# Optimization experiments

Measured on AMD Instinct MI355X. Metric: run time of the kernel, lower is better.

## Reference

```python
import jax, jax.numpy as jnp
import numpy as np

N, E, IN, H0, H1 = 50000, 1600000, 64, 64, 128


def _gcn(h, W, b, row, col):
    # PyG GCNConv, add_self_loops=False, unit edge weights:
    # out[col] += d^{-1/2}[row] * d^{-1/2}[col] * (h @ W)[row]; bias added after aggregation
    n = h.shape[0]
    deg = jnp.zeros((n,), h.dtype).at[col].add(jnp.ones((row.shape[0],), h.dtype))
    dinv = jnp.where(deg > 0, jax.lax.rsqrt(jnp.maximum(deg, 1e-12)), 0.0)
    norm = (dinv[row] * dinv[col])[:, None]  # [E,1]
    m = h @ W  # transform before propagate (small GEMM)
    out = jnp.zeros((n, W.shape[1]), h.dtype).at[col].add(norm * m[row])
    return out + b


def _bn(h, g, b):
    # BatchNorm1d training-mode math (biased variance), eps=1e-5
    mu = h.mean(0)
    var = ((h - mu) ** 2).mean(0)
    return g * (h - mu) * jax.lax.rsqrt(var + 1e-5) + b


def _san(h):
    return jnp.nan_to_num(h, nan=0.0, posinf=100.0, neginf=-100.0)


def _slice(x, ei, W0, b0, W1, b1, res1, g0, be0, g1, be1):
    row, col = ei[0], ei[1]
    # layer 0: conv -> bn -> relu -> (dropout=eval identity) -> residual (Identity, 64==64) -> nan_to_num
    h1 = _san(jax.nn.relu(_bn(_gcn(x, W0, b0, row, col), g0, be0)) + x)
    # layer 1 (last): conv -> bn -> residual (Linear proj 64->128, no bias) -> nan_to_num
    h2 = _san(_bn(_gcn(h1, W1, b1, row, col), g1, be1) + h1 @ res1)
    return h2


def setup_inputs() -> dict:
    k = jax.random.split(jax.random.key(0), 16)
    f = lambda kk, sh, s: jax.random.normal(kk, sh, jnp.float32) * s
    return {
        "x": f(k[0], (N, IN), 1.0),
        "edge_index0": jax.random.randint(k[1], (2, E), 0, N),
        "edge_index1": jax.random.randint(k[2], (2, E), 0, N),
        "w0_s0": f(k[3], (IN, H0), 0.1), "b0_s0": jnp.zeros((H0,), jnp.float32),
        "w1_s0": f(k[4], (H0, H1), 0.1), "b1_s0": jnp.zeros((H1,), jnp.float32),
        "res1_s0": f(k[5], (H0, H1), 0.1),
        "w0_s1": f(k[6], (IN, H0), 0.1), "b0_s1": jnp.zeros((H0,), jnp.float32),
        "w1_s1": f(k[7], (H0, H1), 0.1), "b1_s1": jnp.zeros((H1,), jnp.float32),
        "res1_s1": f(k[8], (H0, H1), 0.1),
        "bn_g0": jnp.ones((H0,), jnp.float32), "bn_b0": jnp.zeros((H0,), jnp.float32),
        "bn_g1": jnp.ones((H1,), jnp.float32), "bn_b1": jnp.zeros((H1,), jnp.float32),
        "fc1_w": f(k[9], (2 * H1, H1), 0.1), "fc1_b": jnp.zeros((H1,), jnp.float32),
        "fc2_w": f(k[10], (H1, 2), 0.1), "fc2_b": jnp.zeros((2,), jnp.float32),
    }


def reference(x, edge_index0, edge_index1,
              w0_s0, b0_s0, w1_s0, b1_s0, res1_s0,
              w0_s1, b0_s1, w1_s1, b1_s1, res1_s1,
              bn_g0, bn_b0, bn_g1, bn_b1,
              fc1_w, fc1_b, fc2_w, fc2_b):
    out0 = _slice(x, edge_index0, w0_s0, b0_s0, w1_s0, b1_s0, res1_s0, bn_g0, bn_b0, bn_g1, bn_b1)
    out1 = _slice(x, edge_index1, w0_s1, b0_s1, w1_s1, b1_s1, res1_s1, bn_g0, bn_b0, bn_g1, bn_b1)
    combined = jnp.concatenate([out0, out1], axis=1)  # [N, 2*H1]
    h = jax.nn.relu(combined @ fc1_w + fc1_b)  # dropout is eval-mode identity
    logits = h @ fc2_w + fc2_b
    return logits, jax.nn.softmax(logits, axis=1)
```

## Files before the change

kernel.cpp:

```cpp
#include <hip/hip_runtime.h>
#include <hip/hip_bf16.h>
#include <math.h>


typedef short v8s __attribute__((ext_vector_type(8)));
typedef float f32x4 __attribute__((ext_vector_type(4)));

#define BSTRIDE 10240

__device__ __forceinline__ float sanf(float v) {
    if (v != v) return 0.f;
    if (isinf(v)) return v > 0.f ? 100.f : -100.f;
    return v;
}

__device__ __forceinline__ unsigned short bf16of(float v) {
    __hip_bfloat16 h = __float2bfloat16(v);
    return *(unsigned short*)&h;
}
__device__ __forceinline__ unsigned pack2(float lo, float hi) {
    return (unsigned)bf16of(lo) | ((unsigned)bf16of(hi) << 16);
}
__device__ __forceinline__ float uflo(unsigned u) { return __uint_as_float(u << 16); }
__device__ __forceinline__ float ufhi(unsigned u) { return __uint_as_float(u & 0xFFFF0000u); }
__device__ __forceinline__ float fofbf16(unsigned short u) {
    return __uint_as_float(((unsigned)u) << 16);
}

__device__ __forceinline__ void packone(const float* __restrict__ src, unsigned* __restrict__ dst,
                                        int L, int Khalf, int F) {
    int c = L / Khalf, kp = L - c * Khalf;
    dst[L] = pack2(src[(2 * kp) * F + c], src[(2 * kp + 1) * F + c]);
}

__global__ __launch_bounds__(256) void prep_kernel(const float* __restrict__ w0_0,
                                                   const float* __restrict__ w0_1,
                                                   const float* __restrict__ w1_0,
                                                   const float* __restrict__ w1_1,
                                                   const float* __restrict__ r_0,
                                                   const float* __restrict__ r_1,
                                                   const float* __restrict__ fc1,
                                                   const float* __restrict__ x,
                                                   unsigned* __restrict__ wpk,
                                                   int* __restrict__ bcnt,
                                                   float* __restrict__ sums,
                                                   unsigned short* __restrict__ xb, int n64) {
    int gid = blockIdx.x * 256 + threadIdx.x;
    if (gid < 512) bcnt[gid] = 0;
    if (gid < 8192) sums[gid] = 0.f;
    if (gid < 2048)       packone(w0_0, wpk + 0,     gid - 0,     32, 64);
    else if (gid < 4096)  packone(w0_1, wpk + 2048,  gid - 2048,  32, 64);
    else if (gid < 8192)  packone(w1_0, wpk + 4096,  gid - 4096,  32, 128);
    else if (gid < 12288) packone(w1_1, wpk + 8192,  gid - 8192,  32, 128);
    else if (gid < 16384) packone(r_0,  wpk + 12288, gid - 12288, 32, 128);
    else if (gid < 20480) packone(r_1,  wpk + 16384, gid - 16384, 32, 128);
    else if (gid < 36864) packone(fc1,  wpk + 20480, gid - 20480, 128, 128);
    if (gid < n64) xb[gid] = bf16of(x[gid]);
}


__global__ __launch_bounds__(512) void kC_bin(const int* __restrict__ ei0,
                                              const int* __restrict__ ei1,
                                              int* __restrict__ bcnt,
                                              unsigned* __restrict__ binned,
                                              int E, int n) {
    __shared__ int cnt[512];
    __shared__ int base[512];
    int t = threadIdx.x;
    cnt[t] = 0;
    int E2 = 2 * E;
    int e0 = blockIdx.x * 8192;
    unsigned pk[16];
    int bk[16];
    __syncthreads();
#pragma unroll
    for (int j = 0; j < 16; ++j) {
        int ge = e0 + t + j * 512;
        bk[j] = -1;
        if (ge < E2) {
            int slice = ge >= E;
            const int* ei = slice ? ei1 : ei0;
            int e = ge - slice * E;
            int col = ei[E + e], row = ei[e];
            int gcol = slice * n + col;
            bk[j] = gcol >> 8;
            pk[j] = (unsigned)row | (((unsigned)gcol & 255u) << 16);
            atomicAdd(&cnt[bk[j]], 1);
        }
    }
    __syncthreads();
    {
        int c = cnt[t];
        base[t] = c ? atomicAdd(&bcnt[t], c) : 0;
    }
    __syncthreads();
    cnt[t] = 0;
    __syncthreads();
#pragma unroll
    for (int j = 0; j < 16; ++j) {
        if (bk[j] >= 0) {
            int loc = atomicAdd(&cnt[bk[j]], 1);
            int off = base[bk[j]] + loc;
            if (off < BSTRIDE) binned[(size_t)bk[j] * BSTRIDE + off] = pk[j];
        }
    }
}

__global__ __launch_bounds__(256) void kB_scan(const int* __restrict__ bcnt,
                                               int* __restrict__ bstart, int NB) {
    __shared__ int tmp[256];
    int t = threadIdx.x, carry = 0;
    for (int bse = 0; bse < NB; bse += 256) {
        int i = bse + t;
        int v = (i < NB) ? bcnt[i] : 0;
        tmp[t] = v;
        __syncthreads();
        for (int off = 1; off < 256; off <<= 1) {
            int u = (t >= off) ? tmp[t - off] : 0;
            __syncthreads();
            tmp[t] += u;
            __syncthreads();
        }
        if (i < NB) bstart[i] = tmp[t] - v + carry;
        carry += tmp[255];
        __syncthreads();
    }
    if (t == 0) bstart[NB] = carry;
}

__global__ __launch_bounds__(512) void kD_build(const unsigned* __restrict__ binned,
                                                const int* __restrict__ bstart,
                                                int* __restrict__ rowptr,
                                                float* __restrict__ dinv,
                                                unsigned short* __restrict__ csr,
                                                int n2, int NB) {
    __shared__ int cnt[256];
    __shared__ int scn[256];
    __shared__ int cur[256];
    int b = blockIdx.x, t = threadIdx.x;
    int s = bstart[b], e = bstart[b + 1];
    int m = e - s;
    const unsigned* seg = binned + (size_t)b * BSTRIDE;
    if (t < 256) cnt[t] = 0;
    __syncthreads();
    for (int i = t; i < m; i += 512) atomicAdd(&cnt[(seg[i] >> 16) & 255], 1);
    __syncthreads();
    int v = (t < 256) ? cnt[t] : 0;
    if (t < 256) scn[t] = v;
    __syncthreads();
    for (int off = 1; off < 256; off <<= 1) {
        int u = (t < 256 && t >= off) ? scn[t - off] : 0;
        __syncthreads();
        if (t < 256) scn[t] += u;
        __syncthreads();
    }
    if (t < 256) {
        int excl = scn[t] - v;
        int gcol = b * 256 + t;
        if (gcol < n2) {
            rowptr[gcol] = s + excl;
            dinv[gcol] = v > 0 ? rsqrtf((float)v) : 0.f;
        }
        cur[t] = excl;
    }
    __syncthreads();
    for (int i = t; i < m; i += 512) {
        unsigned p = seg[i];
        int cl = (p >> 16) & 255;
        int pos = s + atomicAdd(&cur[cl], 1);
        csr[pos] = (unsigned short)(p & 0xFFFFu);
    }
    if (b == 0 && t == 0) rowptr[n2] = bstart[NB];
}

template <int F>
__global__ __launch_bounds__(256) void gg_kernel(const int* __restrict__ rowptr,
                                                 const unsigned short* __restrict__ csr,
                                                 const unsigned short* __restrict__ mtab,
                                                 size_t slice_stride,
                                                 const float* __restrict__ dinv,
                                                 const unsigned* __restrict__ WT0,
                                                 const unsigned* __restrict__ WT1,
                                                 unsigned short* __restrict__ Cb,
                                                 float* __restrict__ sums_base,
                                                 int roff, int n) {
    constexpr int NC = F / 16;
    __shared__ unsigned As32[64 * 36];
    __shared__ float ls[2 * F];
    int BPS = (n + 63) >> 6;
    int slice = blockIdx.x >= BPS;
    int sb = blockIdx.x - slice * BPS;
    int row0 = slice * n + sb * 64;
    int rows = min(64, n - sb * 64);
    for (int i = threadIdx.x; i < 2 * F; i += 256) ls[i] = 0.f;
    int w = threadIdx.x >> 6, lane = threadIdx.x & 63;
    int l = lane & 7;
    const unsigned short* mb = mtab + slice_stride * slice;
    const float* dsrc = dinv + slice * n;
#pragma unroll
    for (int p = 0; p < 2; ++p) {
        int nl = 16 * w + p * 8 + (lane >> 3);
        float a0 = 0.f, a1 = 0.f, a2 = 0.f, a3 = 0.f, a4 = 0.f, a5 = 0.f, a6 = 0.f, a7 = 0.f;
        if (nl < rows) {
            int node = row0 + nl;
            int s = rowptr[node], e = rowptr[node + 1];
            int b = s;
            for (; b + 8 <= e; b += 8) {
                int idx = csr[b + l];
                float wsrc = dsrc[idx];
                uint4 u[8];
                float ws[8];
#pragma unroll
                for (int j = 0; j < 8; ++j) {
                    int r = __shfl(idx, j, 8);
                    ws[j] = __shfl(wsrc, j, 8);
                    u[j] = *(const uint4*)&mb[(size_t)r * 64 + l * 8];
                }
#pragma unroll
                for (int j = 0; j < 8; ++j) {
                    a0 = fmaf(ws[j], uflo(u[j].x), a0);
                    a1 = fmaf(ws[j], ufhi(u[j].x), a1);
                    a2 = fmaf(ws[j], uflo(u[j].y), a2);
                    a3 = fmaf(ws[j], ufhi(u[j].y), a3);
                    a4 = fmaf(ws[j], uflo(u[j].z), a4);
                    a5 = fmaf(ws[j], ufhi(u[j].z), a5);
                    a6 = fmaf(ws[j], uflo(u[j].w), a6);
                    a7 = fmaf(ws[j], ufhi(u[j].w), a7);
                }
            }
            if (b < e) {
                int cntn = e - b;
                int idx = (b + l < e) ? (int)csr[b + l] : 0;
                float wsrc = dsrc[idx];
                for (int j = 0; j < cntn; ++j) {
                    int r = __shfl(idx, j, 8);
                    float wj = __shfl(wsrc, j, 8);
                    uint4 u = *(const uint4*)&mb[(size_t)r * 64 + l * 8];
                    a0 = fmaf(wj, uflo(u.x), a0);
                    a1 = fmaf(wj, ufhi(u.x), a1);
                    a2 = fmaf(wj, uflo(u.y), a2);
                    a3 = fmaf(wj, ufhi(u.y), a3);
                    a4 = fmaf(wj, uflo(u.z), a4);
                    a5 = fmaf(wj, ufhi(u.z), a5);
                    a6 = fmaf(wj, uflo(u.w), a6);
                    a7 = fmaf(wj, ufhi(u.w), a7);
                }
            }
            float d = dinv[node];
            a0 *= d; a1 *= d; a2 *= d; a3 *= d;
            a4 *= d; a5 *= d; a6 *= d; a7 *= d;
        }
        uint4 o;
        o.x = pack2(a0, a1);
        o.y = pack2(a2, a3);
        o.z = pack2(a4, a5);
        o.w = pack2(a6, a7);
        *(uint4*)&As32[nl * 36 + l * 4] = o;
    }
    __syncthreads();
    const unsigned* WT = slice ? WT1 : WT0;
    int q = lane >> 4, ln = lane & 15;
    v8s af0 = *(const v8s*)&As32[(16 * w + ln) * 36 + q * 4];
    v8s af1 = *(const v8s*)&As32[(16 * w + ln) * 36 + 16 + q * 4];
    f32x4 acc[NC];
#pragma unroll
    for (int ct = 0; ct < NC; ++ct) acc[ct] = {0.f, 0.f, 0.f, 0.f};
#pragma unroll
    for (int ct = 0; ct < NC; ++ct) {
        v8s b0 = *(const v8s*)&WT[(ct * 16 + ln) * 32 + q * 4];
        v8s b1 = *(const v8s*)&WT[(ct * 16 + ln) * 32 + 16 + q * 4];
        acc[ct] = __builtin_amdgcn_mfma_f32_16x16x32_bf16(af0, b0, acc[ct], 0, 0, 0);
        acc[ct] = __builtin_amdgcn_mfma_f32_16x16x32_bf16(af1, b1, acc[ct], 0, 0, 0);
    }
#pragma unroll
    for (int ct = 0; ct < NC; ++ct) {
        float s1 = 0.f, s2 = 0.f;
#pragma unroll
        for (int i = 0; i < 4; ++i) {
            int r = 16 * w + q * 4 + i;
            if (r < rows) {
                float v = acc[ct][i];
                Cb[(size_t)(row0 + r) * F + ct * 16 + ln] = bf16of(v);
                s1 += v;
                s2 += v * v;
            }
        }
        s1 += __shfl_xor(s1, 16); s1 += __shfl_xor(s1, 32);
        s2 += __shfl_xor(s2, 16); s2 += __shfl_xor(s2, 32);
        if (q == 0) {
            atomicAdd(&ls[ct * 16 + ln], s1);
            atomicAdd(&ls[F + ct * 16 + ln], s2);
        }
    }
    __syncthreads();
    if (threadIdx.x < F) {
        float* dst = sums_base + (blockIdx.x & 7) * 1024 + roff + slice * 2 * F;
        unsafeAtomicAdd(&dst[threadIdx.x], ls[threadIdx.x]);
        unsafeAtomicAdd(&dst[F + threadIdx.x], ls[F + threadIdx.x]);
    }
}


__global__ __launch_bounds__(256) void apply0_kernel(const unsigned short* __restrict__ t0b,
                                                     const float* __restrict__ x,
                                                     const float* __restrict__ sums_base,
                                                     int roff,
                                                     const float* __restrict__ g,
                                                     const float* __restrict__ be,
                                                     unsigned short* __restrict__ h1b,
                                                     int n64, int n) {
    __shared__ float sc[128];
    int i0 = blockIdx.x * 256;
    int slice = i0 >= n64;
    int t = threadIdx.x;
    if (t < 64) {
        float s1 = 0.f, s2 = 0.f;
#pragma unroll
        for (int r = 0; r < 8; ++r) {
            const float* src = sums_base + r * 1024 + roff + slice * 128;
            s1 += src[t];
            s2 += src[64 + t];
        }
        float inv_n = 1.0f / (float)n;
        float mu = s1 * inv_n;
        float var = fmaxf(s2 * inv_n - mu * mu, 0.f);
        float scale = g[t] * rsqrtf(var + 1e-5f);
        sc[t] = scale;
        sc[64 + t] = be[t] - mu * scale;
    }
    __syncthreads();
    int i = i0 + t;
    int f = i & 63;
    float v = fmaf(fofbf16(t0b[i]), sc[f], sc[64 + f]);
    v = fmaxf(v, 0.f) + x[i - slice * n64];
    h1b[i] = bf16of(sanf(v));
}

__global__ __launch_bounds__(256) void mfma_apply1(const unsigned short* __restrict__ h1b,
                                                   const unsigned short* __restrict__ Tb,
                                                   const unsigned* __restrict__ RT0,
                                                   const unsigned* __restrict__ RT1,
                                                   const float* __restrict__ sums_base,
                                                   const float* __restrict__ g,
                                                   const float* __restrict__ be,
                                                   unsigned short* __restrict__ comb, int n) {
    __shared__ float sc[256];
    int BPS = (n + 63) >> 6;
    int slice = blockIdx.x >= BPS;
    int sb = blockIdx.x - slice * BPS;
    int row0 = slice * n + sb * 64;
    int rows = min(64, n - sb * 64);
    int t = threadIdx.x;
    if (t < 128) {
        float s1 = 0.f, s2 = 0.f;
#pragma unroll
        for (int r = 0; r < 8; ++r) {
            const float* src = sums_base + r * 1024 + slice * 256;
            s1 += src[t];
            s2 += src[128 + t];
        }
        float inv_n = 1.0f / (float)n;
        float mu = s1 * inv_n;
        float var = fmaxf(s2 * inv_n - mu * mu, 0.f);
        float scale = g[t] * rsqrtf(var + 1e-5f);
        sc[t] = scale;
        sc[128 + t] = be[t] - mu * scale;
    }
    __syncthreads();
    const unsigned* WT = slice ? RT1 : RT0;
    int w = t >> 6, lane = t & 63, q = lane >> 4, ln = lane & 15;
    const unsigned* A32 = (const unsigned*)h1b;
    size_t arow = (size_t)(row0 + 16 * w + ln) * 32;
    v8s af0 = *(const v8s*)&A32[arow + q * 4];
    v8s af1 = *(const v8s*)&A32[arow + 16 + q * 4];
    f32x4 acc[8];
#pragma unroll
    for (int ct = 0; ct < 8; ++ct) acc[ct] = {0.f, 0.f, 0.f, 0.f};
#pragma unroll
    for (int ct = 0; ct < 8; ++ct) {
        v8s b0 = *(const v8s*)&WT[(ct * 16 + ln) * 32 + q * 4];
        v8s b1 = *(const v8s*)&WT[(ct * 16 + ln) * 32 + 16 + q * 4];
        acc[ct] = __builtin_amdgcn_mfma_f32_16x16x32_bf16(af0, b0, acc[ct], 0, 0, 0);
        acc[ct] = __builtin_amdgcn_mfma_f32_16x16x32_bf16(af1, b1, acc[ct], 0, 0, 0);
    }
#pragma unroll
    for (int ct = 0; ct < 8; ++ct) {
        int c = ct * 16 + ln;
        float scale = sc[c], shift = sc[128 + c];
#pragma unroll
        for (int i = 0; i < 4; ++i) {
            int r = 16 * w + q * 4 + i;
            if (r >= rows) continue;
            int row = row0 + r;
            float tv = fofbf16(Tb[(size_t)row * 128 + c]);
            float o = sanf(fmaf(tv, scale, shift) + acc[ct][i]);
            comb[(size_t)(row - slice * n) * 256 + slice * 128 + c] = bf16of(o);
        }
    }
}

__global__ __launch_bounds__(256) void mfma_head_fc2(const unsigned short* __restrict__ comb,
                                                     const unsigned* __restrict__ FT,
                                                     const float* __restrict__ bias,
                                                     const float* __restrict__ w2,
                                                     const float* __restrict__ b2,
                                                     float* __restrict__ out, int n) {
    int row0 = blockIdx.x * 64;
    int rows = min(64, n - row0);
    int w = threadIdx.x >> 6, lane = threadIdx.x & 63, q = lane >> 4, ln = lane & 15;
    const unsigned* A32 = (const unsigned*)comb;
    size_t arow = (size_t)(row0 + 16 * w + ln) * 128;
    f32x4 acc[8];
#pragma unroll
    for (int ct = 0; ct < 8; ++ct) acc[ct] = {0.f, 0.f, 0.f, 0.f};
#pragma unroll
    for (int kt = 0; kt < 4; ++kt) {
        v8s af0 = *(const v8s*)&A32[arow + kt * 32 + q * 4];
        v8s af1 = *(const v8s*)&A32[arow + kt * 32 + 16 + q * 4];
#pragma unroll
        for (int ct = 0; ct < 8; ++ct) {
            v8s b0 = *(const v8s*)&FT[(ct * 16 + ln) * 128 + kt * 32 + q * 4];
            v8s b1 = *(const v8s*)&FT[(ct * 16 + ln) * 128 + kt * 32 + 16 + q * 4];
            acc[ct] = __builtin_amdgcn_mfma_f32_16x16x32_bf16(af0, b0, acc[ct], 0, 0, 0);
            acc[ct] = __builtin_amdgcn_mfma_f32_16x16x32_bf16(af1, b1, acc[ct], 0, 0, 0);
        }
    }
    float p0[4] = {0.f, 0.f, 0.f, 0.f}, p1[4] = {0.f, 0.f, 0.f, 0.f};
#pragma unroll
    for (int ct = 0; ct < 8; ++ct) {
        int c = ct * 16 + ln;
        float bi = bias[c];
        float w20 = w2[c * 2], w21 = w2[c * 2 + 1];
#pragma unroll
        for (int i = 0; i < 4; ++i) {
            float h = fmaxf(acc[ct][i] + bi, 0.f);
            p0[i] = fmaf(h, w20, p0[i]);
            p1[i] = fmaf(h, w21, p1[i]);
        }
    }
#pragma unroll
    for (int i = 0; i < 4; ++i) {
#pragma unroll
        for (int msk = 1; msk < 16; msk <<= 1) {
            p0[i] += __shfl_xor(p0[i], msk);
            p1[i] += __shfl_xor(p1[i], msk);
        }
    }
    if (ln == 0) {
        float bb0 = b2[0], bb1 = b2[1];
#pragma unroll
        for (int i = 0; i < 4; ++i) {
            int r = 16 * w + q * 4 + i;
            if (r >= rows) continue;
            int R = row0 + r;
            float l0 = p0[i] + bb0, l1 = p1[i] + bb1;
            float mx = fmaxf(l0, l1);
            float e0 = expf(l0 - mx), e1 = expf(l1 - mx);
            float inv = 1.0f / (e0 + e1);
            out[(size_t)R * 2] = l0;
            out[(size_t)R * 2 + 1] = l1;
            out[(size_t)2 * n + R * 2] = e0 * inv;
            out[(size_t)2 * n + R * 2 + 1] = e1 * inv;
        }
    }
}

static inline int cdiv(int a, int b) { return (a + b - 1) / b; }

extern "C" void kernel_launch(void* const* d_in, const int* in_sizes, int n_in,
                              void* d_out, int out_size, void* d_ws, size_t ws_size,
                              hipStream_t stream) {
    const float* x       = (const float*)d_in[0];
    const int*   ei0     = (const int*)d_in[1];
    const int*   ei1     = (const int*)d_in[2];
    const float* w0_s0   = (const float*)d_in[3];
    const float* w1_s0   = (const float*)d_in[5];
    const float* res1_s0 = (const float*)d_in[7];
    const float* w0_s1   = (const float*)d_in[8];
    const float* w1_s1   = (const float*)d_in[10];
    const float* res1_s1 = (const float*)d_in[12];
    const float* bn_g0   = (const float*)d_in[13];
    const float* bn_b0   = (const float*)d_in[14];
    const float* bn_g1   = (const float*)d_in[15];
    const float* bn_b1   = (const float*)d_in[16];
    const float* fc1_w   = (const float*)d_in[17];
    const float* fc1_b   = (const float*)d_in[18];
    const float* fc2_w   = (const float*)d_in[19];
    const float* fc2_b   = (const float*)d_in[20];
    float* out = (float*)d_out;

    int n = in_sizes[0] / 64;
    int E = in_sizes[1] / 2;
    int n2 = 2 * n, E2 = 2 * E;
    int n64 = n * 64;
    int NB = cdiv(n2, 256);
    int BPS = cdiv(n, 64);

    unsigned short* Tb   = (unsigned short*)d_ws;
    unsigned short* h1b  = Tb + (size_t)n2 * 128;
    unsigned short* comb = h1b + (size_t)n2 * 64;
    unsigned short* xb   = comb + (size_t)n * 256;
    float* dinv = (float*)(xb + (size_t)n * 64);
    float* sums = dinv + n2;
    unsigned* wpk = (unsigned*)(sums + 8192);
    unsigned short* csr = (unsigned short*)(wpk + 36864);
    int* rowptr = (int*)(csr + (size_t)E2);
    int* bcnt   = rowptr + (n2 + 1);
    int* bstart = bcnt + 512;
    unsigned short* t0b = Tb;
    unsigned* binned = (unsigned*)comb;
    unsigned* w0T0 = wpk + 0,    *w0T1 = wpk + 2048;
    unsigned* w1T0 = wpk + 4096, *w1T1 = wpk + 8192;
    unsigned* rT0  = wpk + 12288,*rT1  = wpk + 16384;
    unsigned* fT   = wpk + 20480;

    prep_kernel<<<cdiv(n64, 256), 256, 0, stream>>>(w0_s0, w0_s1, w1_s0, w1_s1,
                                                    res1_s0, res1_s1, fc1_w, x,
                                                    wpk, bcnt, sums, xb, n64);
    kC_bin<<<cdiv(E2, 8192), 512, 0, stream>>>(ei0, ei1, bcnt, binned, E, n);
    kB_scan<<<1, 256, 0, stream>>>(bcnt, bstart, NB);
    kD_build<<<NB, 512, 0, stream>>>(binned, bstart, rowptr, dinv, csr, n2, NB);

    gg_kernel<64><<<2 * BPS, 256, 0, stream>>>(rowptr, csr, xb, 0, dinv,
                                               w0T0, w0T1, t0b, sums, 512, n);
    apply0_kernel<<<2 * n64 / 256, 256, 0, stream>>>(t0b, x, sums, 512, bn_g0, bn_b0,
                                                     h1b, n64, n);

    gg_kernel<128><<<2 * BPS, 256, 0, stream>>>(rowptr, csr, h1b, (size_t)n * 64, dinv,
                                                w1T0, w1T1, Tb, sums, 0, n);
    mfma_apply1<<<2 * BPS, 256, 0, stream>>>(h1b, Tb, rT0, rT1, sums, bn_g1, bn_b1,
                                             comb, n);

    mfma_head_fc2<<<BPS, 256, 0, stream>>>(comb, fT, fc1_b, fc2_w, fc2_b, out, n);
}
```

Before: 408.3 us.

## Split fused gather+GEMM kernel into separate gather and MFMA GEMM kernels

```diff
diff --git a/kernel.cpp b/kernel.cpp
--- a/kernel.cpp
+++ b/kernel.cpp
@@ -173,95 +173,95 @@
     if (b == 0 && t == 0) rowptr[n2] = bstart[NB];
 }
 
+__global__ __launch_bounds__(256) void gatherw_kernel(const int* __restrict__ rowptr,
+                                                      const unsigned short* __restrict__ csr,
+                                                      const unsigned short* __restrict__ mtab,
+                                                      size_t slice_stride,
+                                                      const float* __restrict__ dinv,
+                                                      unsigned short* __restrict__ outb,
+                                                      int n, int n2) {
+    int gid = blockIdx.x * 256 + threadIdx.x;
+    int node = gid >> 3;
+    if (node >= n2) return;
+    int l = threadIdx.x & 7;
+    int slice = node >= n;
+    const unsigned short* mb = mtab + slice_stride * slice;
+    const float* dsrc = dinv + (size_t)slice * n;
+    int s = rowptr[node], e = rowptr[node + 1];
+    float a0 = 0.f, a1 = 0.f, a2 = 0.f, a3 = 0.f, a4 = 0.f, a5 = 0.f, a6 = 0.f, a7 = 0.f;
+    int b = s;
+    for (; b + 8 <= e; b += 8) {
+        int idx = csr[b + l];
+        float wsrc = dsrc[idx];
+        uint4 u[8];
+        float ws[8];
+#pragma unroll
+        for (int j = 0; j < 8; ++j) {
+            int r = __shfl(idx, j, 8);
+            ws[j] = __shfl(wsrc, j, 8);
+            u[j] = *(const uint4*)&mb[(size_t)r * 64 + l * 8];
+        }
+#pragma unroll
+        for (int j = 0; j < 8; ++j) {
+            a0 = fmaf(ws[j], uflo(u[j].x), a0);
+            a1 = fmaf(ws[j], ufhi(u[j].x), a1);
+            a2 = fmaf(ws[j], uflo(u[j].y), a2);
+            a3 = fmaf(ws[j], ufhi(u[j].y), a3);
+            a4 = fmaf(ws[j], uflo(u[j].z), a4);
+            a5 = fmaf(ws[j], ufhi(u[j].z), a5);
+            a6 = fmaf(ws[j], uflo(u[j].w), a6);
+            a7 = fmaf(ws[j], ufhi(u[j].w), a7);
+        }
+    }
+    if (b < e) {
+        int cntn = e - b;
+        int idx = (b + l < e) ? (int)csr[b + l] : 0;
+        float wsrc = dsrc[idx];
+        for (int j = 0; j < cntn; ++j) {
+            int r = __shfl(idx, j, 8);
+            float wj = __shfl(wsrc, j, 8);
+            uint4 u = *(const uint4*)&mb[(size_t)r * 64 + l * 8];
+            a0 = fmaf(wj, uflo(u.x), a0);
+            a1 = fmaf(wj, ufhi(u.x), a1);
+            a2 = fmaf(wj, uflo(u.y), a2);
+            a3 = fmaf(wj, ufhi(u.y), a3);
+            a4 = fmaf(wj, uflo(u.z), a4);
+            a5 = fmaf(wj, ufhi(u.z), a5);
+            a6 = fmaf(wj, uflo(u.w), a6);
+            a7 = fmaf(wj, ufhi(u.w), a7);
+        }
+    }
+    float d = dinv[node];
+    uint4 o;
+    o.x = pack2(a0 * d, a1 * d);
+    o.y = pack2(a2 * d, a3 * d);
+    o.z = pack2(a4 * d, a5 * d);
+    o.w = pack2(a6 * d, a7 * d);
+    *(uint4*)&outb[(size_t)node * 64 + l * 8] = o;
+}
+
+
 template <int F>
-__global__ __launch_bounds__(256) void gg_kernel(const int* __restrict__ rowptr,
-                                                 const unsigned short* __restrict__ csr,
-                                                 const unsigned short* __restrict__ mtab,
-                                                 size_t slice_stride,
-                                                 const float* __restrict__ dinv,
-                                                 const unsigned* __restrict__ WT0,
-                                                 const unsigned* __restrict__ WT1,
-                                                 unsigned short* __restrict__ Cb,
-                                                 float* __restrict__ sums_base,
-                                                 int roff, int n) {
+__global__ __launch_bounds__(256) void mfma_gemmb(const unsigned short* __restrict__ Ab,
+                                                  const unsigned* __restrict__ WT0,
+                                                  const unsigned* __restrict__ WT1,
+                                                  unsigned short* __restrict__ Cb,
+                                                  float* __restrict__ sums_base,
+                                                  int roff, int n) {
     constexpr int NC = F / 16;
-    __shared__ unsigned As32[64 * 36];
     __shared__ float ls[2 * F];
     int BPS = (n + 63) >> 6;
     int slice = blockIdx.x >= BPS;
     int sb = blockIdx.x - slice * BPS;
+    const unsigned* WT = slice ? WT1 : WT0;
     int row0 = slice * n + sb * 64;
     int rows = min(64, n - sb * 64);
     for (int i = threadIdx.x; i < 2 * F; i += 256) ls[i] = 0.f;
-    int w = threadIdx.x >> 6, lane = threadIdx.x & 63;
-    int l = lane & 7;
-    const unsigned short* mb = mtab + slice_stride * slice;
-    const float* dsrc = dinv + slice * n;
-#pragma unroll
-    for (int p = 0; p < 2; ++p) {
-        int nl = 16 * w + p * 8 + (lane >> 3);
-        float a0 = 0.f, a1 = 0.f, a2 = 0.f, a3 = 0.f, a4 = 0.f, a5 = 0.f, a6 = 0.f, a7 = 0.f;
-        if (nl < rows) {
-            int node = row0 + nl;
-            int s = rowptr[node], e = rowptr[node + 1];
-            int b = s;
-            for (; b + 8 <= e; b += 8) {
-                int idx = csr[b + l];
-                float wsrc = dsrc[idx];
-                uint4 u[8];
-                float ws[8];
-#pragma unroll
-                for (int j = 0; j < 8; ++j) {
-                    int r = __shfl(idx, j, 8);
-                    ws[j] = __shfl(wsrc, j, 8);
-                    u[j] = *(const uint4*)&mb[(size_t)r * 64 + l * 8];
-                }
-#pragma unroll
-                for (int j = 0; j < 8; ++j) {
-                    a0 = fmaf(ws[j], uflo(u[j].x), a0);
-                    a1 = fmaf(ws[j], ufhi(u[j].x), a1);
-                    a2 = fmaf(ws[j], uflo(u[j].y), a2);
-                    a3 = fmaf(ws[j], ufhi(u[j].y), a3);
-                    a4 = fmaf(ws[j], uflo(u[j].z), a4);
-                    a5 = fmaf(ws[j], ufhi(u[j].z), a5);
-                    a6 = fmaf(ws[j], uflo(u[j].w), a6);
-                    a7 = fmaf(ws[j], ufhi(u[j].w), a7);
-                }
-            }
-            if (b < e) {
-                int cntn = e - b;
-                int idx = (b + l < e) ? (int)csr[b + l] : 0;
-                float wsrc = dsrc[idx];
-                for (int j = 0; j < cntn; ++j) {
-                    int r = __shfl(idx, j, 8);
-                    float wj = __shfl(wsrc, j, 8);
-                    uint4 u = *(const uint4*)&mb[(size_t)r * 64 + l * 8];
-                    a0 = fmaf(wj, uflo(u.x), a0);
-                    a1 = fmaf(wj, ufhi(u.x), a1);
-                    a2 = fmaf(wj, uflo(u.y), a2);
-                    a3 = fmaf(wj, ufhi(u.y), a3);
-                    a4 = fmaf(wj, uflo(u.z), a4);
-                    a5 = fmaf(wj, ufhi(u.z), a5);
-                    a6 = fmaf(wj, uflo(u.w), a6);
-                    a7 = fmaf(wj, ufhi(u.w), a7);
-                }
-            }
-            float d = dinv[node];
-            a0 *= d; a1 *= d; a2 *= d; a3 *= d;
-            a4 *= d; a5 *= d; a6 *= d; a7 *= d;
-        }
-        uint4 o;
-        o.x = pack2(a0, a1);
-        o.y = pack2(a2, a3);
-        o.z = pack2(a4, a5);
-        o.w = pack2(a6, a7);
-        *(uint4*)&As32[nl * 36 + l * 4] = o;
-    }
-    __syncthreads();
-    const unsigned* WT = slice ? WT1 : WT0;
-    int q = lane >> 4, ln = lane & 15;
-    v8s af0 = *(const v8s*)&As32[(16 * w + ln) * 36 + q * 4];
-    v8s af1 = *(const v8s*)&As32[(16 * w + ln) * 36 + 16 + q * 4];
+    int w = threadIdx.x >> 6, lane = threadIdx.x & 63, q = lane >> 4, ln = lane & 15;
+    const unsigned* A32 = (const unsigned*)Ab;
+    size_t arow = (size_t)(row0 + 16 * w + ln) * 32;
+    v8s af0 = *(const v8s*)&A32[arow + q * 4];
+    v8s af1 = *(const v8s*)&A32[arow + 16 + q * 4];
     f32x4 acc[NC];
 #pragma unroll
     for (int ct = 0; ct < NC; ++ct) acc[ct] = {0.f, 0.f, 0.f, 0.f};
@@ -272,6 +272,7 @@
         acc[ct] = __builtin_amdgcn_mfma_f32_16x16x32_bf16(af0, b0, acc[ct], 0, 0, 0);
         acc[ct] = __builtin_amdgcn_mfma_f32_16x16x32_bf16(af1, b1, acc[ct], 0, 0, 0);
     }
+    __syncthreads();
 #pragma unroll
     for (int ct = 0; ct < NC; ++ct) {
         float s1 = 0.f, s2 = 0.f;
@@ -499,7 +500,8 @@
     unsigned short* Tb   = (unsigned short*)d_ws;
     unsigned short* h1b  = Tb + (size_t)n2 * 128;
     unsigned short* comb = h1b + (size_t)n2 * 64;
-    unsigned short* xb   = comb + (size_t)n * 256;
+    unsigned short* Gb   = comb + (size_t)n * 256;
+    unsigned short* xb   = Gb + (size_t)n2 * 64;
     float* dinv = (float*)(xb + (size_t)n * 64);
     float* sums = dinv + n2;
     unsigned* wpk = (unsigned*)(sums + 8192);
@@ -521,13 +523,14 @@
     kB_scan<<<1, 256, 0, stream>>>(bcnt, bstart, NB);
     kD_build<<<NB, 512, 0, stream>>>(binned, bstart, rowptr, dinv, csr, n2, NB);
 
-    gg_kernel<64><<<2 * BPS, 256, 0, stream>>>(rowptr, csr, xb, 0, dinv,
-                                               w0T0, w0T1, t0b, sums, 512, n);
+    gatherw_kernel<<<cdiv(n2 * 8, 256), 256, 0, stream>>>(rowptr, csr, xb, 0, dinv, Gb, n, n2);
+    mfma_gemmb<64><<<2 * BPS, 256, 0, stream>>>(Gb, w0T0, w0T1, t0b, sums, 512, n);
     apply0_kernel<<<2 * n64 / 256, 256, 0, stream>>>(t0b, x, sums, 512, bn_g0, bn_b0,
                                                      h1b, n64, n);
 
-    gg_kernel<128><<<2 * BPS, 256, 0, stream>>>(rowptr, csr, h1b, (size_t)n * 64, dinv,
-                                                w1T0, w1T1, Tb, sums, 0, n);
+    gatherw_kernel<<<cdiv(n2 * 8, 256), 256, 0, stream>>>(rowptr, csr, h1b, (size_t)n * 64,
+                                                          dinv, Gb, n, n2);
+    mfma_gemmb<128><<<2 * BPS, 256, 0, stream>>>(Gb, w1T0, w1T1, Tb, sums, 0, n);
     mfma_apply1<<<2 * BPS, 256, 0, stream>>>(h1b, Tb, rT0, rT1, sums, bn_g1, bn_b1,
                                              comb, n);
 
```

Result: faster. 399.4 us (-2.2%).
